# Performance work log

Hardware: AMD Instinct MI355X
Metric: run time of the kernel (lower is better)

## Reference

```python
import jax, jax.numpy as jnp
import numpy as np

B = 1024      # number of subgraphs in the batch
S = 128       # nodes per subgraph (last node is the anchor)
N = B * S     # total nodes
E = 2_097_152 # total edges (avg degree 16)
F_IN = 300
F_OUT = 64


def setup_inputs() -> dict:
    key = jax.random.key(0)
    kx, kg, ks, kd, kw = jax.random.split(key, 5)
    in_feat = jax.random.normal(kx, (N, F_IN), dtype=jnp.float32)
    # edges constrained within subgraphs (batched DGL graph semantics)
    gid = jax.random.randint(kg, (E,), 0, B)
    src = (gid * S + jax.random.randint(ks, (E,), 0, S)).astype(jnp.int32)
    dst = (gid * S + jax.random.randint(kd, (E,), 0, S)).astype(jnp.int32)
    W = jax.random.normal(kw, (F_IN, F_OUT), dtype=jnp.float32) * 0.05
    b = jnp.zeros((F_OUT,), dtype=jnp.float32)
    prelu_a = jnp.float32(0.25)  # nn.PReLU default single parameter
    return {"in_feat": in_feat, "W": W, "b": b, "prelu_a": prelu_a,
            "src": src, "dst": dst}


def reference(in_feat, W, b, prelu_a, src, dst):
    ones = jnp.ones((E,), dtype=jnp.float32)
    deg_out = jnp.clip(jax.ops.segment_sum(ones, src, num_segments=N), 1.0)
    deg_in = jnp.clip(jax.ops.segment_sum(ones, dst, num_segments=N), 1.0)
    # GraphConv norm='both': weight first (in_feats > out_feats), then SpMM
    x = in_feat * jax.lax.rsqrt(deg_out)[:, None]
    h = x @ W                                   # [N, F_OUT]
    agg = jax.ops.segment_sum(h[src], dst, num_segments=N)
    h = agg * jax.lax.rsqrt(deg_in)[:, None] + b
    # PReLU
    h = jnp.where(h > 0, h, prelu_a * h)
    # ragged per-subgraph mean over all nodes except the last (anchor)
    node_idx = jnp.arange(N)
    seg = node_idx // S                          # subgraph id per node
    not_anchor = ((node_idx % S) != (S - 1)).astype(h.dtype)
    pool_sum = jax.ops.segment_sum(h * not_anchor[:, None], seg, num_segments=B)
    subgraph_pool_emb = pool_sum / jnp.float32(S - 1)
    anchor_out = h[(jnp.arange(B) + 1) * S - 1]  # last node of each subgraph
    return subgraph_pool_emb, anchor_out
```

## Files before the change

### kernel.cpp

```cpp
#include <hip/hip_runtime.h>
#include <hip/hip_bf16.h>

#define NNODES 131072
#define NEDGES 2097152
#define BSUB   1024
#define SSUB   128
#define FIN    300
#define FOUT   64
#define NCHUNK 256
#define CHEDGE 8192

typedef __attribute__((ext_vector_type(8))) short short8;
typedef __attribute__((ext_vector_type(8))) unsigned short ushort8;
typedef __attribute__((ext_vector_type(4))) float f32x4;

__device__ inline unsigned short f2bfbits(float f) {
    union { __hip_bfloat16 h; unsigned short u; } cv;
    cv.h = __float2bfloat16(f);
    return cv.u;
}
__device__ inline float bf2f(unsigned short b) {
    return __uint_as_float(((unsigned)b) << 16);
}

__global__ __launch_bounds__(256) void prep_w_kernel(const float* __restrict__ W,
                                                     short* __restrict__ wfrag,
                                                     int* __restrict__ gcnt) {
    int idx = blockIdx.x * 256 + threadIdx.x;
    if (idx < BSUB) gcnt[idx] = 0;
    if (idx >= 2560) return;
    int ct   = idx / 640;
    int rem  = idx % 640;
    int kt   = rem / 64;
    int lane = rem % 64;
    int col  = ct * 16 + (lane & 15);
    int kb   = kt * 32 + (lane >> 4) * 8;
#pragma unroll
    for (int e = 0; e < 8; ++e) {
        int k = kb + e;
        float v = (k < FIN) ? W[(size_t)k * FOUT + col] : 0.f;
        wfrag[(size_t)idx * 8 + e] = (short)f2bfbits(v);
    }
}

__global__ __launch_bounds__(256) void bucket_gemm_kernel(const int* __restrict__ src,
                                                          const int* __restrict__ dst,
                                                          int* __restrict__ gcnt,
                                                          unsigned short* __restrict__ bkt,
                                                          const float* __restrict__ x,
                                                          const short* __restrict__ wfrag,
                                                          unsigned short* __restrict__ hb) {
    if (blockIdx.x < NCHUNK) {
        __shared__ int hist[BSUB];
        const int cb = blockIdx.x;
        const int t = threadIdx.x;
        for (int i = t; i < BSUB; i += 256) hist[i] = 0;
        __syncthreads();
        const int4* sp = (const int4*)(src + (size_t)cb * CHEDGE);
        for (int i = t; i < CHEDGE / 4; i += 256) {
            int4 v = sp[i];
            atomicAdd(&hist[v.x >> 7], 1);
            atomicAdd(&hist[v.y >> 7], 1);
            atomicAdd(&hist[v.z >> 7], 1);
            atomicAdd(&hist[v.w >> 7], 1);
        }
        __syncthreads();
        for (int i = t; i < BSUB; i += 256) {
            int c = hist[i];
            hist[i] = c ? atomicAdd(&gcnt[i], c) : 0;
        }
        __syncthreads();
        const int4* dp = (const int4*)(dst + (size_t)cb * CHEDGE);
        for (int i = t; i < CHEDGE / 4; i += 256) {
            int4 s4 = sp[i], d4 = dp[i];
#pragma unroll
            for (int k = 0; k < 4; ++k) {
                int s = (k == 0) ? s4.x : (k == 1) ? s4.y : (k == 2) ? s4.z : s4.w;
                int d = (k == 0) ? d4.x : (k == 1) ? d4.y : (k == 2) ? d4.z : d4.w;
                int g = s >> 7;
                int r = atomicAdd(&hist[g], 1);
                bkt[((size_t)g << 12) + r] = (unsigned short)(((s & 127) << 7) | (d & 127));
            }
        }
        return;
    }
    const int wave = threadIdx.x >> 6;
    const int lane = threadIdx.x & 63;
    const int rowbase = ((blockIdx.x - NCHUNK) * 4 + wave) * 16;
    const int arow = rowbase + (lane & 15);
    const int kgrp = lane >> 4;

    f32x4 acc[4];
#pragma unroll
    for (int c = 0; c < 4; ++c) acc[c] = (f32x4){0.f, 0.f, 0.f, 0.f};

    const float* ap = x + (size_t)arow * FIN + kgrp * 8;
#pragma unroll
    for (int kt = 0; kt < 9; ++kt) {
        f32x4 lo = *(const f32x4*)(ap + kt * 32);
        f32x4 hi = *(const f32x4*)(ap + kt * 32 + 4);
        short8 afr;
        afr[0] = (short)f2bfbits(lo[0]); afr[1] = (short)f2bfbits(lo[1]);
        afr[2] = (short)f2bfbits(lo[2]); afr[3] = (short)f2bfbits(lo[3]);
        afr[4] = (short)f2bfbits(hi[0]); afr[5] = (short)f2bfbits(hi[1]);
        afr[6] = (short)f2bfbits(hi[2]); afr[7] = (short)f2bfbits(hi[3]);
#pragma unroll
        for (int ct = 0; ct < 4; ++ct) {
            short8 bfr = *(const short8*)(wfrag + ((size_t)(ct * 10 + kt) * 64 + lane) * 8);
            acc[ct] = __builtin_amdgcn_mfma_f32_16x16x32_bf16(afr, bfr, acc[ct], 0, 0, 0);
        }
    }
    {
        short8 afr;
#pragma unroll
        for (int e = 0; e < 8; ++e) {
            int k = 288 + kgrp * 8 + e;
            float v = (k < FIN) ? x[(size_t)arow * FIN + k] : 0.f;
            afr[e] = (short)f2bfbits(v);
        }
#pragma unroll
        for (int ct = 0; ct < 4; ++ct) {
            short8 bfr = *(const short8*)(wfrag + ((size_t)(ct * 10 + 9) * 64 + lane) * 8);
            acc[ct] = __builtin_amdgcn_mfma_f32_16x16x32_bf16(afr, bfr, acc[ct], 0, 0, 0);
        }
    }
    const int orow = rowbase + (lane >> 4) * 4;
    const int colb = lane & 15;
#pragma unroll
    for (int ct = 0; ct < 4; ++ct)
#pragma unroll
        for (int r = 0; r < 4; ++r)
            hb[(size_t)(orow + r) * FOUT + ct * 16 + colb] = f2bfbits(acc[ct][r]);
}

__global__ __launch_bounds__(256) void agg_pool_kernel(const unsigned short* __restrict__ hb,
                                                       const unsigned short* __restrict__ bkt,
                                                       const int* __restrict__ gcnt,
                                                       const float* __restrict__ bias,
                                                       const float* __restrict__ prelu,
                                                       float* __restrict__ out) {
    __shared__ unsigned short hl[SSUB][FOUT];
    __shared__ unsigned char  es[SSUB][64];
    __shared__ int   din[SSUB];
    __shared__ int   dout[SSUB];
    __shared__ float rout[SSUB];
    __shared__ float ps[4][FOUT];

    const int g = blockIdx.x;
    const int t = threadIdx.x;
    const int lane = t & 63;
    const int w = t >> 6;

    {
        const ushort8* hsrc = (const ushort8*)(hb + (size_t)g * SSUB * FOUT);
        ushort8* hdst = (ushort8*)&hl[0][0];
        for (int i = t; i < 1024; i += 256) hdst[i] = hsrc[i];
    }
    if (t < SSUB) { din[t] = 0; dout[t] = 0; }
    __syncthreads();

    const int cnt = gcnt[g];
    const unsigned short* eb = bkt + ((size_t)g << 12);

    for (int i = t; i < cnt; i += 256) {
        unsigned e = eb[i];
        int s = e >> 7, d = e & 127;
        int r = atomicAdd(&din[d], 1);
        es[d][r & 63] = (unsigned char)s;
        atomicAdd(&dout[s], 1);
    }
    __syncthreads();
    if (t < SSUB) rout[t] = rsqrtf((float)max(dout[t], 1));
    __syncthreads();

    const float bv = bias[lane];
    const float a = prelu[0];
    float pool = 0.f;
#pragma unroll 4
    for (int ii = 0; ii < 32; ++ii) {
        int d = w + 4 * ii;
        int cd = min(din[d], 64);
        float accv = 0.f;
        const unsigned* ew = (const unsigned*)&es[d][0];
        int nw = (cd + 3) >> 2;
        for (int p = 0; p < nw; ++p) {
            unsigned wd = ew[p];
            int rem = cd - p * 4;
#pragma unroll
            for (int b = 0; b < 4; ++b) {
                if (b < rem) {
                    int s = (wd >> (8 * b)) & 127;
                    accv += bf2f(hl[s][lane]) * rout[s];
                }
            }
        }
        float v = accv * rsqrtf((float)max(din[d], 1)) + bv;
        v = (v > 0.f) ? v : a * v;
        if (d == SSUB - 1)
            out[(size_t)(BSUB + g) * FOUT + lane] = v;
        else
            pool += v;
    }
    ps[w][lane] = pool;
    __syncthreads();
    if (w == 0) {
        float s = (ps[0][lane] + ps[1][lane]) + (ps[2][lane] + ps[3][lane]);
        out[(size_t)g * FOUT + lane] = s * (1.0f / 127.0f);
    }
}

extern "C" void kernel_launch(void* const* d_in, const int* in_sizes, int n_in,
                              void* d_out, int out_size, void* d_ws, size_t ws_size,
                              hipStream_t stream) {
    const float* in_feat = (const float*)d_in[0];
    const float* W       = (const float*)d_in[1];
    const float* bias    = (const float*)d_in[2];
    const float* prelu   = (const float*)d_in[3];
    const int*   src     = (const int*)d_in[4];
    const int*   dst     = (const int*)d_in[5];
    float* out = (float*)d_out;

    char* ws = (char*)d_ws;
    int*            gcnt  = (int*)(ws);
    short*          wfrag = (short*)(ws + 65536);
    unsigned short* bkt   = (unsigned short*)(ws + (1u << 20));
    unsigned short* hb    = (unsigned short*)(ws + (16u << 20));

    hipLaunchKernelGGL(prep_w_kernel,     dim3(10),                 dim3(256), 0, stream, W, wfrag, gcnt);
    hipLaunchKernelGGL(bucket_gemm_kernel,dim3(NCHUNK + NNODES/64), dim3(256), 0, stream,
                       src, dst, gcnt, bkt, in_feat, wfrag, hb);
    hipLaunchKernelGGL(agg_pool_kernel,   dim3(BSUB),               dim3(256), 0, stream, hb, bkt, gcnt, bias, prelu, out);
}
```

Measured before the change: 120.9 us.

## Stage GEMM input rows through LDS with direct global-to-LDS loads and coalesced stores

The GEMM part now loads each 64-row block of in_feat into two swizzled 32KB LDS buffers with global_load_lds, so the global reads are coalesced instead of strided per-lane row reads. The last K tiles come from registers loaded up front. The bf16 output tile is staged in LDS so it can be written with 16-byte vector stores. In exchange the kernel reserves 64KB of shared memory, which applies to the histogram blocks too and can lower occupancy.

```diff
diff --git a/kernel.cpp b/kernel.cpp
--- a/kernel.cpp
+++ b/kernel.cpp
@@ -21,6 +21,13 @@
 }
 __device__ inline float bf2f(unsigned short b) {
     return __uint_as_float(((unsigned)b) << 16);
+}
+
+__device__ inline void gload_lds16(const float* g, void* l) {
+    __builtin_amdgcn_global_load_lds(
+        (const __attribute__((address_space(1))) unsigned int*)g,
+        (__attribute__((address_space(3))) unsigned int*)l,
+        16, 0, 0);
 }
 
 __global__ __launch_bounds__(256) void prep_w_kernel(const float* __restrict__ W,
@@ -50,8 +57,10 @@
                                                           const float* __restrict__ x,
                                                           const short* __restrict__ wfrag,
                                                           unsigned short* __restrict__ hb) {
+    __shared__ __align__(16) char smem[65536];
+
     if (blockIdx.x < NCHUNK) {
-        __shared__ int hist[BSUB];
+        int* hist = (int*)smem;
         const int cb = blockIdx.x;
         const int t = threadIdx.x;
         for (int i = t; i < BSUB; i += 256) hist[i] = 0;
@@ -84,21 +93,59 @@
         }
         return;
     }
+    char* bufA = smem;
+    char* bufB = smem + 32768;
+
     const int wave = threadIdx.x >> 6;
     const int lane = threadIdx.x & 63;
-    const int rowbase = ((blockIdx.x - NCHUNK) * 4 + wave) * 16;
-    const int arow = rowbase + (lane & 15);
-    const int kgrp = lane >> 4;
+    const int rowbase = (blockIdx.x - NCHUNK) * 64;
+    const int rl = wave * 16 + (lane & 15);
+    const int kg = lane >> 4;
+    const int arow = rowbase + rl;
+
+    const float* arp = x + (size_t)arow * FIN;
+    f32x4 t8a = *(const f32x4*)(arp + 256 + kg * 8);
+    f32x4 t8b = *(const f32x4*)(arp + 256 + kg * 8 + 4);
+    f32x4 t9a = (f32x4){0.f, 0.f, 0.f, 0.f};
+    f32x4 t9b = (f32x4){0.f, 0.f, 0.f, 0.f};
+    if (kg == 0) {
+        t9a = *(const f32x4*)(arp + 288);
+        t9b = *(const f32x4*)(arp + 292);
+    } else if (kg == 1) {
+        t9a = *(const f32x4*)(arp + 296);
+    }
+
+#pragma unroll
+    for (int i = wave; i < 32; i += 4) {
+        int o = i * 1024 + lane * 16;
+        int row = o >> 9;
+        int c = o & 511;
+        int csrc = c ^ ((row & 7) << 4);
+        gload_lds16(x + (size_t)(rowbase + row) * FIN + (csrc >> 2), bufA + i * 1024);
+    }
+#pragma unroll
+    for (int i = wave; i < 32; i += 4) {
+        int o = i * 1024 + lane * 16;
+        int row = o >> 9;
+        int c = o & 511;
+        int csrc = c ^ ((row & 7) << 4);
+        gload_lds16(x + (size_t)(rowbase + row) * FIN + 128 + (csrc >> 2), bufB + i * 1024);
+    }
 
     f32x4 acc[4];
 #pragma unroll
     for (int c = 0; c < 4; ++c) acc[c] = (f32x4){0.f, 0.f, 0.f, 0.f};
 
-    const float* ap = x + (size_t)arow * FIN + kgrp * 8;
-#pragma unroll
-    for (int kt = 0; kt < 9; ++kt) {
-        f32x4 lo = *(const f32x4*)(ap + kt * 32);
-        f32x4 hi = *(const f32x4*)(ap + kt * 32 + 4);
+    const int sw = (rl & 7) << 4;
+
+    __syncthreads();
+
+#pragma unroll
+    for (int kt = 0; kt < 8; ++kt) {
+        const char* buf = (kt < 4) ? bufA : bufB;
+        int c0 = (kt & 3) * 128 + kg * 32;
+        f32x4 lo = *(const f32x4*)(buf + rl * 512 + (c0 ^ sw));
+        f32x4 hi = *(const f32x4*)(buf + rl * 512 + ((c0 + 16) ^ sw));
         short8 afr;
         afr[0] = (short)f2bfbits(lo[0]); afr[1] = (short)f2bfbits(lo[1]);
         afr[2] = (short)f2bfbits(lo[2]); afr[3] = (short)f2bfbits(lo[3]);
@@ -110,27 +157,36 @@
             acc[ct] = __builtin_amdgcn_mfma_f32_16x16x32_bf16(afr, bfr, acc[ct], 0, 0, 0);
         }
     }
+#pragma unroll
+    for (int kt = 8; kt < 10; ++kt) {
+        f32x4 lo = (kt == 8) ? t8a : t9a;
+        f32x4 hi = (kt == 8) ? t8b : t9b;
+        short8 afr;
+        afr[0] = (short)f2bfbits(lo[0]); afr[1] = (short)f2bfbits(lo[1]);
+        afr[2] = (short)f2bfbits(lo[2]); afr[3] = (short)f2bfbits(lo[3]);
+        afr[4] = (short)f2bfbits(hi[0]); afr[5] = (short)f2bfbits(hi[1]);
+        afr[6] = (short)f2bfbits(hi[2]); afr[7] = (short)f2bfbits(hi[3]);
+#pragma unroll
+        for (int ct = 0; ct < 4; ++ct) {
+            short8 bfr = *(const short8*)(wfrag + ((size_t)(ct * 10 + kt) * 64 + lane) * 8);
+            acc[ct] = __builtin_amdgcn_mfma_f32_16x16x32_bf16(afr, bfr, acc[ct], 0, 0, 0);
+        }
+    }
+
     {
-        short8 afr;
-#pragma unroll
-        for (int e = 0; e < 8; ++e) {
-            int k = 288 + kgrp * 8 + e;
-            float v = (k < FIN) ? x[(size_t)arow * FIN + k] : 0.f;
-            afr[e] = (short)f2bfbits(v);
-        }
-#pragma unroll
-        for (int ct = 0; ct < 4; ++ct) {
-            short8 bfr = *(const short8*)(wfrag + ((size_t)(ct * 10 + 9) * 64 + lane) * 8);
-            acc[ct] = __builtin_amdgcn_mfma_f32_16x16x32_bf16(afr, bfr, acc[ct], 0, 0, 0);
-        }
-    }
-    const int orow = rowbase + (lane >> 4) * 4;
-    const int colb = lane & 15;
-#pragma unroll
-    for (int ct = 0; ct < 4; ++ct)
-#pragma unroll
-        for (int r = 0; r < 4; ++r)
-            hb[(size_t)(orow + r) * FOUT + ct * 16 + colb] = f2bfbits(acc[ct][r]);
+        unsigned short* st = (unsigned short*)(bufB + wave * 8192);
+        const int lrow = (lane >> 4) * 4;
+        const int colb = lane & 15;
+#pragma unroll
+        for (int ct = 0; ct < 4; ++ct)
+#pragma unroll
+            for (int r = 0; r < 4; ++r)
+                st[(lrow + r) * FOUT + ct * 16 + colb] = f2bfbits(acc[ct][r]);
+        const ushort8* sv = (const ushort8*)st;
+        ushort8* hout = (ushort8*)(hb + (size_t)(rowbase + wave * 16) * FOUT);
+        hout[lane] = sv[lane];
+        hout[lane + 64] = sv[lane + 64];
+    }
 }
 
 __global__ __launch_bounds__(256) void agg_pool_kernel(const unsigned short* __restrict__ hb,
```

Result: faster. 111.2 us (-8.1%).

## Split bucket and GEMM kernels, stage W fragments in LDS, vectorize stores

Applied to the files above, without the earlier changes.

Splits the fused bucketing/GEMM kernel into two separate launches. The GEMM kernel now copies the 40 KB W fragment array into LDS once per block, vectorizes the tail K load, and stages output tiles through LDS so each wave writes its 16x64 bf16 rows as coalesced 16-byte stores. The goal is to cut redundant global W reads and scattered 2-byte stores. The costs are an extra kernel launch, the loss of overlap between bucketing and GEMM, and about 48 KB of LDS per block, which may limit occupancy.

```diff
diff --git a/kernel.cpp b/kernel.cpp
--- a/kernel.cpp
+++ b/kernel.cpp
@@ -43,58 +43,67 @@
     }
 }
 
-__global__ __launch_bounds__(256) void bucket_gemm_kernel(const int* __restrict__ src,
-                                                          const int* __restrict__ dst,
-                                                          int* __restrict__ gcnt,
-                                                          unsigned short* __restrict__ bkt,
-                                                          const float* __restrict__ x,
-                                                          const short* __restrict__ wfrag,
-                                                          unsigned short* __restrict__ hb) {
-    if (blockIdx.x < NCHUNK) {
-        __shared__ int hist[BSUB];
-        const int cb = blockIdx.x;
-        const int t = threadIdx.x;
-        for (int i = t; i < BSUB; i += 256) hist[i] = 0;
-        __syncthreads();
-        const int4* sp = (const int4*)(src + (size_t)cb * CHEDGE);
-        for (int i = t; i < CHEDGE / 4; i += 256) {
-            int4 v = sp[i];
-            atomicAdd(&hist[v.x >> 7], 1);
-            atomicAdd(&hist[v.y >> 7], 1);
-            atomicAdd(&hist[v.z >> 7], 1);
-            atomicAdd(&hist[v.w >> 7], 1);
-        }
-        __syncthreads();
-        for (int i = t; i < BSUB; i += 256) {
-            int c = hist[i];
-            hist[i] = c ? atomicAdd(&gcnt[i], c) : 0;
-        }
-        __syncthreads();
-        const int4* dp = (const int4*)(dst + (size_t)cb * CHEDGE);
-        for (int i = t; i < CHEDGE / 4; i += 256) {
-            int4 s4 = sp[i], d4 = dp[i];
-#pragma unroll
-            for (int k = 0; k < 4; ++k) {
-                int s = (k == 0) ? s4.x : (k == 1) ? s4.y : (k == 2) ? s4.z : s4.w;
-                int d = (k == 0) ? d4.x : (k == 1) ? d4.y : (k == 2) ? d4.z : d4.w;
-                int g = s >> 7;
-                int r = atomicAdd(&hist[g], 1);
-                bkt[((size_t)g << 12) + r] = (unsigned short)(((s & 127) << 7) | (d & 127));
-            }
-        }
-        return;
-    }
+__global__ __launch_bounds__(256) void bucket_kernel(const int* __restrict__ src,
+                                                     const int* __restrict__ dst,
+                                                     int* __restrict__ gcnt,
+                                                     unsigned short* __restrict__ bkt) {
+    __shared__ int hist[BSUB];
+    const int cb = blockIdx.x;
+    const int t = threadIdx.x;
+    for (int i = t; i < BSUB; i += 256) hist[i] = 0;
+    __syncthreads();
+    const int4* sp = (const int4*)(src + (size_t)cb * CHEDGE);
+    for (int i = t; i < CHEDGE / 4; i += 256) {
+        int4 v = sp[i];
+        atomicAdd(&hist[v.x >> 7], 1);
+        atomicAdd(&hist[v.y >> 7], 1);
+        atomicAdd(&hist[v.z >> 7], 1);
+        atomicAdd(&hist[v.w >> 7], 1);
+    }
+    __syncthreads();
+    for (int i = t; i < BSUB; i += 256) {
+        int c = hist[i];
+        hist[i] = c ? atomicAdd(&gcnt[i], c) : 0;
+    }
+    __syncthreads();
+    const int4* dp = (const int4*)(dst + (size_t)cb * CHEDGE);
+    for (int i = t; i < CHEDGE / 4; i += 256) {
+        int4 s4 = sp[i], d4 = dp[i];
+#pragma unroll
+        for (int k = 0; k < 4; ++k) {
+            int s = (k == 0) ? s4.x : (k == 1) ? s4.y : (k == 2) ? s4.z : s4.w;
+            int d = (k == 0) ? d4.x : (k == 1) ? d4.y : (k == 2) ? d4.z : d4.w;
+            int g = s >> 7;
+            int r = atomicAdd(&hist[g], 1);
+            bkt[((size_t)g << 12) + r] = (unsigned short)(((s & 127) << 7) | (d & 127));
+        }
+    }
+}
+
+__global__ __launch_bounds__(256) void gemm_kernel(const float* __restrict__ x,
+                                                   const short* __restrict__ wfrag,
+                                                   unsigned short* __restrict__ hb) {
+    __shared__ short wl[20480];
+    __shared__ unsigned short st[4][16][FOUT];
+
+    {
+        const ushort8* srcv = (const ushort8*)wfrag;
+        ushort8* dstv = (ushort8*)wl;
+        for (int i = threadIdx.x; i < 2560; i += 256) dstv[i] = srcv[i];
+    }
+    __syncthreads();
+
     const int wave = threadIdx.x >> 6;
     const int lane = threadIdx.x & 63;
-    const int rowbase = ((blockIdx.x - NCHUNK) * 4 + wave) * 16;
+    const int rowbase = (blockIdx.x * 4 + wave) * 16;
     const int arow = rowbase + (lane & 15);
     const int kgrp = lane >> 4;
+    const float* ap = x + (size_t)arow * FIN + kgrp * 8;
 
     f32x4 acc[4];
 #pragma unroll
     for (int c = 0; c < 4; ++c) acc[c] = (f32x4){0.f, 0.f, 0.f, 0.f};
 
-    const float* ap = x + (size_t)arow * FIN + kgrp * 8;
 #pragma unroll
     for (int kt = 0; kt < 9; ++kt) {
         f32x4 lo = *(const f32x4*)(ap + kt * 32);
@@ -106,31 +115,45 @@
         afr[6] = (short)f2bfbits(hi[2]); afr[7] = (short)f2bfbits(hi[3]);
 #pragma unroll
         for (int ct = 0; ct < 4; ++ct) {
-            short8 bfr = *(const short8*)(wfrag + ((size_t)(ct * 10 + kt) * 64 + lane) * 8);
+            short8 bfr = *(const short8*)(wl + ((ct * 10 + kt) * 64 + lane) * 8);
             acc[ct] = __builtin_amdgcn_mfma_f32_16x16x32_bf16(afr, bfr, acc[ct], 0, 0, 0);
         }
     }
     {
+        f32x4 t9a = (f32x4){0.f, 0.f, 0.f, 0.f};
+        f32x4 t9b = (f32x4){0.f, 0.f, 0.f, 0.f};
+        const float* arp = x + (size_t)arow * FIN;
+        if (kgrp == 0) {
+            t9a = *(const f32x4*)(arp + 288);
+            t9b = *(const f32x4*)(arp + 292);
+        } else if (kgrp == 1) {
+            t9a = *(const f32x4*)(arp + 296);
+        }
         short8 afr;
-#pragma unroll
-        for (int e = 0; e < 8; ++e) {
-            int k = 288 + kgrp * 8 + e;
-            float v = (k < FIN) ? x[(size_t)arow * FIN + k] : 0.f;
-            afr[e] = (short)f2bfbits(v);
-        }
+        afr[0] = (short)f2bfbits(t9a[0]); afr[1] = (short)f2bfbits(t9a[1]);
+        afr[2] = (short)f2bfbits(t9a[2]); afr[3] = (short)f2bfbits(t9a[3]);
+        afr[4] = (short)f2bfbits(t9b[0]); afr[5] = (short)f2bfbits(t9b[1]);
+        afr[6] = (short)f2bfbits(t9b[2]); afr[7] = (short)f2bfbits(t9b[3]);
 #pragma unroll
         for (int ct = 0; ct < 4; ++ct) {
-            short8 bfr = *(const short8*)(wfrag + ((size_t)(ct * 10 + 9) * 64 + lane) * 8);
+            short8 bfr = *(const short8*)(wl + ((ct * 10 + 9) * 64 + lane) * 8);
             acc[ct] = __builtin_amdgcn_mfma_f32_16x16x32_bf16(afr, bfr, acc[ct], 0, 0, 0);
         }
     }
-    const int orow = rowbase + (lane >> 4) * 4;
-    const int colb = lane & 15;
-#pragma unroll
-    for (int ct = 0; ct < 4; ++ct)
-#pragma unroll
-        for (int r = 0; r < 4; ++r)
-            hb[(size_t)(orow + r) * FOUT + ct * 16 + colb] = f2bfbits(acc[ct][r]);
+
+    {
+        const int lrow = (lane >> 4) * 4;
+        const int colb = lane & 15;
+#pragma unroll
+        for (int ct = 0; ct < 4; ++ct)
+#pragma unroll
+            for (int r = 0; r < 4; ++r)
+                st[wave][lrow + r][ct * 16 + colb] = f2bfbits(acc[ct][r]);
+        const ushort8* sv = (const ushort8*)&st[wave][0][0];
+        ushort8* hout = (ushort8*)(hb + (size_t)rowbase * FOUT);
+        hout[lane] = sv[lane];
+        hout[lane + 64] = sv[lane + 64];
+    }
 }
 
 __global__ __launch_bounds__(256) void agg_pool_kernel(const unsigned short* __restrict__ hb,
@@ -226,8 +249,8 @@
     unsigned short* bkt   = (unsigned short*)(ws + (1u << 20));
     unsigned short* hb    = (unsigned short*)(ws + (16u << 20));
 
-    hipLaunchKernelGGL(prep_w_kernel,     dim3(10),                 dim3(256), 0, stream, W, wfrag, gcnt);
-    hipLaunchKernelGGL(bucket_gemm_kernel,dim3(NCHUNK + NNODES/64), dim3(256), 0, stream,
-                       src, dst, gcnt, bkt, in_feat, wfrag, hb);
-    hipLaunchKernelGGL(agg_pool_kernel,   dim3(BSUB),               dim3(256), 0, stream, hb, bkt, gcnt, bias, prelu, out);
-}
+    hipLaunchKernelGGL(prep_w_kernel,   dim3(10),        dim3(256), 0, stream, W, wfrag, gcnt);
+    hipLaunchKernelGGL(bucket_kernel,   dim3(NCHUNK),    dim3(256), 0, stream, src, dst, gcnt, bkt);
+    hipLaunchKernelGGL(gemm_kernel,     dim3(NNODES/64), dim3(256), 0, stream, in_feat, wfrag, hb);
+    hipLaunchKernelGGL(agg_pool_kernel, dim3(BSUB),      dim3(256), 0, stream, hb, bkt, gcnt, bias, prelu, out);
+}
```

Result: no change. 121.6 us (+0.6%).
